# Kernel optimization log

Hardware: AMD Instinct MI355X
Metric: run time of the kernel (lower is better)

The kernel has to match this reference:

```python
import jax, jax.numpy as jnp
import numpy as np

N_NODES = 100000
N_EDGES = 1600000
D_IN = 128
D_OUT = 32
DROP_P = 0.6
NEG_SLOPE = 0.2


def setup_inputs() -> dict:
    key = jax.random.key(0)
    ks = jax.random.split(key, 10)
    x = jax.random.normal(ks[0], (N_NODES, D_IN), dtype=jnp.float32)
    edge_index = jax.random.randint(ks[1], (2, N_EDGES), 0, N_NODES, dtype=jnp.int32)
    drop_u = jax.random.uniform(ks[2], (N_NODES, D_IN), dtype=jnp.float32)
    s = 1.0 / np.sqrt(D_IN)
    W_src = jax.random.normal(ks[3], (D_IN, D_OUT), dtype=jnp.float32) * s
    W_dst = jax.random.normal(ks[4], (D_IN, D_OUT), dtype=jnp.float32) * s
    att_src = jax.random.normal(ks[5], (D_OUT,), dtype=jnp.float32) * s
    att_dst = jax.random.normal(ks[6], (D_OUT,), dtype=jnp.float32) * s
    bias_gat = jax.random.normal(ks[7], (D_OUT,), dtype=jnp.float32) * 0.01
    W_lin = jax.random.normal(ks[8], (D_OUT, D_OUT), dtype=jnp.float32) / np.sqrt(D_OUT)
    b_lin = jax.random.normal(ks[9], (D_OUT,), dtype=jnp.float32) * 0.01
    return {"x": x, "edge_index": edge_index, "drop_u": drop_u,
            "W_src": W_src, "W_dst": W_dst, "att_src": att_src,
            "att_dst": att_dst, "bias_gat": bias_gat,
            "W_lin": W_lin, "b_lin": b_lin}


def reference(x, edge_index, drop_u, W_src, W_dst, att_src, att_dst,
              bias_gat, W_lin, b_lin):
    n = x.shape[0]
    # F.dropout(x, p=0.6, training=True) with deterministic uniform draws
    keep = (drop_u > DROP_P).astype(x.dtype)
    xd = x * keep / (1.0 - DROP_P)

    # GATConv (heads=1): separate src/dst linear maps
    h_src = xd @ W_src                      # [N, D_OUT]
    h_dst = xd @ W_dst                      # [N, D_OUT]
    a_src = h_src @ att_src                 # [N]
    a_dst = h_dst @ att_dst                 # [N]

    # add_self_loops=True (PyG default)
    loops = jnp.arange(n, dtype=edge_index.dtype)
    src = jnp.concatenate([edge_index[0], loops])   # [E+N]
    dst = jnp.concatenate([edge_index[1], loops])   # [E+N]

    e = a_src[src] + a_dst[dst]                      # per-edge raw score
    e = jnp.where(e > 0, e, NEG_SLOPE * e)           # leaky_relu(0.2)

    # segment softmax over destination-node neighborhoods
    e_max = jax.ops.segment_max(e, dst, num_segments=n)  # every node has a self loop
    e_exp = jnp.exp(e - e_max[dst])
    denom = jax.ops.segment_sum(e_exp, dst, num_segments=n)
    alpha = e_exp / denom[dst]                       # [E+N]

    # scatter-add aggregation of weighted source features
    msg = h_src[src] * alpha[:, None]                # [E+N, D_OUT]
    out = jax.ops.segment_sum(msg, dst, num_segments=n) + bias_gat

    # residual linear + relu + log_softmax
    out = out + out @ W_lin + b_lin
    out = jax.nn.relu(out)
    logp = jax.nn.log_softmax(out, axis=1)
    return logp, alpha
```

## Files before the change

### kernel.cpp

```cpp
#include <hip/hip_runtime.h>
#include <hip/hip_bf16.h>
#include <math.h>

#define D_IN   128
#define D_OUT  32
#define NEG_SLOPE 0.2f
#define DROP_P 0.6f
#define KEEP_SCALE 2.5f

#define NPB     128
#define NB      782
#define CAPB    2816
#define CHUNK   4096
#define BT      512
#define EPT     8
#define SRC_BITS 17
#define SRC_MASK ((1u << SRC_BITS) - 1)

#define SLICES  4
#define NPS     32
#define CAPS    896
#define EPT3    11

typedef __attribute__((ext_vector_type(8))) short fragAB;
typedef __attribute__((ext_vector_type(4))) float fragCD;

__device__ __forceinline__ void atomicMaxF(float* addr, float v) {
    if (v >= 0.0f) atomicMax((int*)addr, __float_as_int(v));
    else           atomicMin((unsigned int*)addr, __float_as_uint(v));
}

__device__ __forceinline__ unsigned pack_bf16(float lo, float hi) {
    __hip_bfloat16 l = __float2bfloat16(lo);
    __hip_bfloat16 h = __float2bfloat16(hi);
    unsigned short lb, hb;
    __builtin_memcpy(&lb, &l, 2);
    __builtin_memcpy(&hb, &h, 2);
    return (unsigned)lb | ((unsigned)hb << 16);
}

__device__ __forceinline__ unsigned short f2bf(float f) {
    __hip_bfloat16 h = __float2bfloat16(f);
    unsigned short u;
    __builtin_memcpy(&u, &h, 2);
    return u;
}

__global__ void k_fold(const float* __restrict__ W_src, const float* __restrict__ W_dst,
                       const float* __restrict__ att_src, const float* __restrict__ att_dst,
                       float* __restrict__ v_src, float* __restrict__ v_dst,
                       int* __restrict__ gcur, uint4* __restrict__ wfrag) {
    int gi = blockIdx.x * blockDim.x + threadIdx.x;
    if (gi < NB) gcur[gi] = gi * CAPB;
    if (gi < 512) {
        int tile = gi >> 8;
        int kb   = (gi >> 6) & 3;
        int lane = gi & 63;
        int grp = lane >> 4, col = lane & 15;
        int kbase = kb * 32 + grp * 8;
        int cidx  = tile * 16 + col;
        unsigned o0 = pack_bf16(W_src[(kbase + 0) * D_OUT + cidx], W_src[(kbase + 1) * D_OUT + cidx]);
        unsigned o1 = pack_bf16(W_src[(kbase + 2) * D_OUT + cidx], W_src[(kbase + 3) * D_OUT + cidx]);
        unsigned o2 = pack_bf16(W_src[(kbase + 4) * D_OUT + cidx], W_src[(kbase + 5) * D_OUT + cidx]);
        unsigned o3 = pack_bf16(W_src[(kbase + 6) * D_OUT + cidx], W_src[(kbase + 7) * D_OUT + cidx]);
        wfrag[gi] = make_uint4(o0, o1, o2, o3);
    }
    if (blockIdx.x == 0) {
        int k = threadIdx.x;
        if (k < D_IN) {
            float s = 0.f, d = 0.f;
            #pragma unroll
            for (int c = 0; c < D_OUT; ++c) {
                s += W_src[k * D_OUT + c] * att_src[c];
                d += W_dst[k * D_OUT + c] * att_dst[c];
            }
            v_src[k] = s;
            v_dst[k] = d;
        }
    }
}

__global__ __launch_bounds__(256) void k_nodes_mfma(
    const float* __restrict__ x, const float* __restrict__ drop_u,
    const uint4* __restrict__ wfrag,
    const float* __restrict__ v_src, const float* __restrict__ v_dst,
    unsigned short* __restrict__ h_bf16,
    float* __restrict__ a_src, float* __restrict__ a_dst,
    int n)
{
    int tid  = threadIdx.x;
    int wv   = tid >> 6;
    int lane = tid & 63;
    int nbase = blockIdx.x * 64 + wv * 16;
    int row = lane & 15, grp = lane >> 4;

    int arow_raw = nbase + row;
    bool aact = arow_raw < n;
    int arow = aact ? arow_raw : (n - 1);
    const float* xr = x      + (size_t)arow * D_IN;
    const float* dr = drop_u + (size_t)arow * D_IN;

    fragCD c0 = {0.f, 0.f, 0.f, 0.f};
    fragCD c1 = {0.f, 0.f, 0.f, 0.f};
    float ps = 0.f, pd = 0.f;

    #pragma unroll
    for (int kb = 0; kb < 4; ++kb) {
        int k0 = kb * 32 + grp * 8;
        float4 xa = *(const float4*)(xr + k0);
        float4 xb = *(const float4*)(xr + k0 + 4);
        float4 da = *(const float4*)(dr + k0);
        float4 db = *(const float4*)(dr + k0 + 4);
        float f0 = da.x > DROP_P ? xa.x * KEEP_SCALE : 0.f;
        float f1 = da.y > DROP_P ? xa.y * KEEP_SCALE : 0.f;
        float f2 = da.z > DROP_P ? xa.z * KEEP_SCALE : 0.f;
        float f3 = da.w > DROP_P ? xa.w * KEEP_SCALE : 0.f;
        float f4 = db.x > DROP_P ? xb.x * KEEP_SCALE : 0.f;
        float f5 = db.y > DROP_P ? xb.y * KEEP_SCALE : 0.f;
        float f6 = db.z > DROP_P ? xb.z * KEEP_SCALE : 0.f;
        float f7 = db.w > DROP_P ? xb.w * KEEP_SCALE : 0.f;

        float4 vs1 = *(const float4*)(v_src + k0);
        float4 vs2 = *(const float4*)(v_src + k0 + 4);
        float4 vd1 = *(const float4*)(v_dst + k0);
        float4 vd2 = *(const float4*)(v_dst + k0 + 4);
        ps += f0 * vs1.x + f1 * vs1.y + f2 * vs1.z + f3 * vs1.w
            + f4 * vs2.x + f5 * vs2.y + f6 * vs2.z + f7 * vs2.w;
        pd += f0 * vd1.x + f1 * vd1.y + f2 * vd1.z + f3 * vd1.w
            + f4 * vd2.x + f5 * vd2.y + f6 * vd2.z + f7 * vd2.w;

        union { unsigned u[4]; fragAB v; } af;
        af.u[0] = pack_bf16(f0, f1);
        af.u[1] = pack_bf16(f2, f3);
        af.u[2] = pack_bf16(f4, f5);
        af.u[3] = pack_bf16(f6, f7);

        fragAB b0 = *reinterpret_cast<const fragAB*>(&wfrag[kb * 64 + lane]);
        fragAB b1 = *reinterpret_cast<const fragAB*>(&wfrag[256 + kb * 64 + lane]);
        c0 = __builtin_amdgcn_mfma_f32_16x16x32_bf16(af.v, b0, c0, 0, 0, 0);
        c1 = __builtin_amdgcn_mfma_f32_16x16x32_bf16(af.v, b1, c1, 0, 0, 0);
    }

    ps += __shfl_xor(ps, 16); ps += __shfl_xor(ps, 32);
    pd += __shfl_xor(pd, 16); pd += __shfl_xor(pd, 32);
    if (grp == 0 && aact) { a_src[arow_raw] = ps; a_dst[arow_raw] = pd; }

    #pragma unroll
    for (int r = 0; r < 4; ++r) {
        int onode = nbase + grp * 4 + r;
        if (onode < n) {
            h_bf16[(size_t)onode * D_OUT + row]      = f2bf(c0[r]);
            h_bf16[(size_t)onode * D_OUT + 16 + row] = f2bf(c1[r]);
        }
    }
}

__global__ __launch_bounds__(256) void k_nodes(
    const float* __restrict__ x, const float* __restrict__ drop_u,
    const float* __restrict__ W_src,
    const float* __restrict__ v_src, const float* __restrict__ v_dst,
    float* __restrict__ h_src, float* __restrict__ a_src, float* __restrict__ a_dst,
    float* __restrict__ e_max, float* __restrict__ denom,
    float* __restrict__ agg, int n, int init_aux)
{
    int gt = blockIdx.x * 256 + threadIdx.x;
    int node_raw = gt >> 2;
    int sub = gt & 3;
    bool act = node_raw < n;
    int node = act ? node_raw : (n - 1);

    const float4* xr4 = (const float4*)(x      + (size_t)node * D_IN) + sub * 8;
    const float4* dr4 = (const float4*)(drop_u + (size_t)node * D_IN) + sub * 8;
    const float*  wb  = W_src + sub * 32 * D_OUT;
    const float4* vsp = (const float4*)v_src + sub * 8;
    const float4* vdp = (const float4*)v_dst + sub * 8;

    float4 xv[8];
    #pragma unroll
    for (int q = 0; q < 8; ++q) {
        float4 xl = xr4[q];
        float4 dl = dr4[q];
        xv[q].x = dl.x > DROP_P ? xl.x * KEEP_SCALE : 0.f;
        xv[q].y = dl.y > DROP_P ? xl.y * KEEP_SCALE : 0.f;
        xv[q].z = dl.z > DROP_P ? xl.z * KEEP_SCALE : 0.f;
        xv[q].w = dl.w > DROP_P ? xl.w * KEEP_SCALE : 0.f;
    }

    float acc[D_OUT];
    #pragma unroll
    for (int c = 0; c < D_OUT; ++c) acc[c] = 0.f;
    float ps = 0.f, pd = 0.f;

    #pragma unroll
    for (int q = 0; q < 8; ++q) {
        float4 vs4 = vsp[q];
        float4 vd4 = vdp[q];
        ps += xv[q].x * vs4.x + xv[q].y * vs4.y + xv[q].z * vs4.z + xv[q].w * vs4.w;
        pd += xv[q].x * vd4.x + xv[q].y * vd4.y + xv[q].z * vd4.z + xv[q].w * vd4.w;
        #pragma unroll
        for (int kk = 0; kk < 4; ++kk) {
            float xk = (kk == 0) ? xv[q].x : (kk == 1) ? xv[q].y : (kk == 2) ? xv[q].z : xv[q].w;
            const float4* wrow = (const float4*)(wb + (q * 4 + kk) * D_OUT);
            #pragma unroll
            for (int c4 = 0; c4 < 8; ++c4) {
                float4 w = wrow[c4];
                acc[c4 * 4 + 0] += xk * w.x;
                acc[c4 * 4 + 1] += xk * w.y;
                acc[c4 * 4 + 2] += xk * w.z;
                acc[c4 * 4 + 3] += xk * w.w;
            }
        }
    }

    #pragma unroll
    for (int c = 0; c < D_OUT; ++c) {
        acc[c] += __shfl_xor(acc[c], 1);
        acc[c] += __shfl_xor(acc[c], 2);
    }
    ps += __shfl_xor(ps, 1); ps += __shfl_xor(ps, 2);
    pd += __shfl_xor(pd, 1); pd += __shfl_xor(pd, 2);

    if (act) {
        if (sub == 0) {
            a_src[node] = ps;
            a_dst[node] = pd;
            if (init_aux) { e_max[node] = -3.0e38f; denom[node] = 0.f; }
        }
        float o[8];
        if (sub == 0) {
            #pragma unroll
            for (int i = 0; i < 8; ++i) o[i] = acc[i];
        } else if (sub == 1) {
            #pragma unroll
            for (int i = 0; i < 8; ++i) o[i] = acc[8 + i];
        } else if (sub == 2) {
            #pragma unroll
            for (int i = 0; i < 8; ++i) o[i] = acc[16 + i];
        } else {
            #pragma unroll
            for (int i = 0; i < 8; ++i) o[i] = acc[24 + i];
        }
        float4* hb = (float4*)(h_src + (size_t)node * D_OUT + sub * 8);
        hb[0] = make_float4(o[0], o[1], o[2], o[3]);
        hb[1] = make_float4(o[4], o[5], o[6], o[7]);
        if (init_aux) {
            float4* ab = (float4*)(agg + (size_t)node * D_OUT + sub * 8);
            ab[0] = make_float4(0.f, 0.f, 0.f, 0.f);
            ab[1] = make_float4(0.f, 0.f, 0.f, 0.f);
        }
    }
}

__global__ __launch_bounds__(BT) void k_binsort(
    const int* __restrict__ ei, int E, int n,
    const float* __restrict__ a_src, const float* __restrict__ a_dst,
    int* __restrict__ gcur, uint2* __restrict__ binned)
{
    __shared__ int A[1024], B[1024];
    __shared__ int excl[NB + 1];
    __shared__ int lcur[NB];
    __shared__ int gpos[NB];
    __shared__ uint2 stage[CHUNK];
    __shared__ unsigned short sbk[CHUNK];

    int tid = threadIdx.x;
    int T   = E + n;
    int base = blockIdx.x * CHUNK;

    for (int k = tid; k < 1024; k += BT) A[k] = 0;
    __syncthreads();

    uint2 rec[EPT];
    int   bk [EPT];
    #pragma unroll
    for (int e = 0; e < EPT; ++e) {
        int i = base + e * BT + tid;
        if (i < T) {
            int s, d;
            if (i < E) { s = ei[i]; d = ei[E + i]; }
            else       { s = d = i - E; }
            int b    = d >> 7;
            int drel = d & 127;
            float sc = a_src[s] + a_dst[d];
            sc = sc > 0.f ? sc : NEG_SLOPE * sc;
            rec[e].x = (unsigned)s | ((unsigned)drel << SRC_BITS);
            rec[e].y = __float_as_uint(expf(sc));
            bk[e]  = b;
            atomicAdd(&A[b], 1);
        } else bk[e] = -1;
    }
    __syncthreads();

    int* cur = A; int* nxt = B;
    for (int off = 1; off < 1024; off <<= 1) {
        for (int k = tid; k < 1024; k += BT) {
            int v = cur[k];
            if (k >= off) v += cur[k - off];
            nxt[k] = v;
        }
        __syncthreads();
        int* t = cur; cur = nxt; nxt = t;
    }

    for (int b = tid; b < NB; b += BT) {
        int e0 = b ? cur[b - 1] : 0;
        excl[b] = e0;
        lcur[b] = e0;
        int c = cur[b] - e0;
        gpos[b] = c ? atomicAdd(&gcur[b], c) : 0;
    }
    if (tid == 0) excl[NB] = cur[NB - 1];
    __syncthreads();

    #pragma unroll
    for (int e = 0; e < EPT; ++e) {
        if (bk[e] >= 0) {
            int slot = atomicAdd(&lcur[bk[e]], 1);
            stage[slot] = rec[e];
            sbk[slot]   = (unsigned short)bk[e];
        }
    }
    __syncthreads();

    int tot = excl[NB];
    for (int j = tid; j < tot; j += BT) {
        int b = sbk[j];
        unsigned gd = (unsigned)(gpos[b] + (j - excl[b]));
        if (gd < (unsigned)(b + 1) * CAPB)
            binned[gd] = stage[j];
    }
}

__global__ __launch_bounds__(256) void k_bucket3(
    const uint2* __restrict__ binned, const int* __restrict__ gcur,
    const unsigned short* __restrict__ h_bf16,
    const float* __restrict__ bias_gat, const float* __restrict__ W_lin,
    const float* __restrict__ b_lin,
    float* __restrict__ inv_out,
    float* __restrict__ io, int n)
{
    __shared__ uint2 grp[CAPS];
    __shared__ int A[NPS];
    __shared__ int ends[NPS];
    __shared__ int ncur[NPS];
    __shared__ float Wl[D_OUT * D_OUT];
    __shared__ float ul[8][D_OUT];

    int tid   = threadIdx.x;
    int lin   = (blockIdx.x & 7) * ((NB * SLICES) >> 3) + (blockIdx.x >> 3);
    int b     = lin >> 2;
    int slice = lin & 3;
    int n0    = b * NPB + slice * NPS;
    int nn    = n - n0; if (nn > NPS) nn = NPS;
    if (nn <= 0) return;

    for (int i = tid; i < D_OUT * D_OUT; i += 256) Wl[i] = W_lin[i];
    if (tid < NPS) A[tid] = 0;
    __syncthreads();

    int cnt = gcur[b] - b * CAPB;
    if (cnt > CAPB) cnt = CAPB;
    const uint2* src = binned + (size_t)b * CAPB;

    uint2 rr[EPT3];
    #pragma unroll
    for (int e = 0; e < EPT3; ++e) {
        int j = tid + e * 256;
        if (j < cnt) {
            uint2 r = src[j];
            rr[e] = r;
            int drel = r.x >> SRC_BITS;
            if ((drel >> 5) == slice) atomicAdd(&A[drel & 31], 1);
        }
    }
    __syncthreads();

    if (tid < NPS) {
        int v = A[tid];
        #pragma unroll
        for (int off = 1; off < NPS; off <<= 1) {
            int u = __shfl_up(v, off, NPS);
            if (tid >= off) v += u;
        }
        ends[tid] = v;
        ncur[tid] = v - A[tid];
    }
    __syncthreads();

    #pragma unroll
    for (int e = 0; e < EPT3; ++e) {
        int j = tid + e * 256;
        if (j < cnt) {
            uint2 r = rr[e];
            int drel = r.x >> SRC_BITS;
            if ((drel >> 5) == slice) {
                int pos = atomicAdd(&ncur[drel & 31], 1);
                if (pos < CAPS) grp[pos] = make_uint2(r.x & SRC_MASK, r.y);
            }
        }
    }
    __syncthreads();

    int g = tid >> 5, lane = tid & 31;
    float bg = bias_gat[lane];
    float bl = b_lin[lane];

    for (int nr = g; nr < nn; nr += 8) {
        int st = nr ? ends[nr - 1] : 0;
        int en = ends[nr];
        if (st > CAPS) st = CAPS;
        if (en > CAPS) en = CAPS;
        int node = n0 + nr;

        float ss = 0.f;
        for (int j = st + lane; j < en; j += 32)
            ss += __uint_as_float(grp[j].y);
        #pragma unroll
        for (int o = 16; o; o >>= 1) ss += __shfl_xor(ss, o);
        float inv = 1.0f / ss;
        if (lane == 0) inv_out[node] = inv;

        float acc0 = 0.f, acc1 = 0.f, acc2 = 0.f, acc3 = 0.f;
        float acc4 = 0.f, acc5 = 0.f, acc6 = 0.f, acc7 = 0.f;
        int j = st;
        for (; j + 7 < en; j += 8) {
            uint2 p0 = grp[j],     p1 = grp[j + 1];
            uint2 p2 = grp[j + 2], p3 = grp[j + 3];
            uint2 p4 = grp[j + 4], p5 = grp[j + 5];
            uint2 p6 = grp[j + 6], p7 = grp[j + 7];
            float h0 = __uint_as_float((unsigned)h_bf16[(p0.x << 5) + lane] << 16);
            float h1 = __uint_as_float((unsigned)h_bf16[(p1.x << 5) + lane] << 16);
            float h2 = __uint_as_float((unsigned)h_bf16[(p2.x << 5) + lane] << 16);
            float h3 = __uint_as_float((unsigned)h_bf16[(p3.x << 5) + lane] << 16);
            float h4 = __uint_as_float((unsigned)h_bf16[(p4.x << 5) + lane] << 16);
            float h5 = __uint_as_float((unsigned)h_bf16[(p5.x << 5) + lane] << 16);
            float h6 = __uint_as_float((unsigned)h_bf16[(p6.x << 5) + lane] << 16);
            float h7 = __uint_as_float((unsigned)h_bf16[(p7.x << 5) + lane] << 16);
            acc0 += h0 * __uint_as_float(p0.y);
            acc1 += h1 * __uint_as_float(p1.y);
            acc2 += h2 * __uint_as_float(p2.y);
            acc3 += h3 * __uint_as_float(p3.y);
            acc4 += h4 * __uint_as_float(p4.y);
            acc5 += h5 * __uint_as_float(p5.y);
            acc6 += h6 * __uint_as_float(p6.y);
            acc7 += h7 * __uint_as_float(p7.y);
        }
        for (; j < en; ++j) {
            uint2 p = grp[j];
            acc0 += __uint_as_float((unsigned)h_bf16[(p.x << 5) + lane] << 16)
                  * __uint_as_float(p.y);
        }

        float u = (((acc0 + acc1) + (acc2 + acc3)) + ((acc4 + acc5) + (acc6 + acc7))) * inv + bg;
        ul[g][lane] = u;
        float r2 = u + bl;
        #pragma unroll 8
        for (int k = 0; k < D_OUT; ++k)
            r2 += ul[g][k] * Wl[k * D_OUT + lane];
        r2 = fmaxf(r2, 0.f);

        float mm = r2;
        #pragma unroll
        for (int o = 16; o; o >>= 1) mm = fmaxf(mm, __shfl_xor(mm, o));
        float e2 = expf(r2 - mm);
        float s2 = e2;
        #pragma unroll
        for (int o = 16; o; o >>= 1) s2 += __shfl_xor(s2, o);
        io[(size_t)node * D_OUT + lane] = r2 - mm - logf(s2);
    }
}

__global__ void k_alpha(const int* __restrict__ ei, int E, int n,
                        const float* __restrict__ a_src, const float* __restrict__ a_dst,
                        const float* __restrict__ inv,
                        float* __restrict__ alpha_out)
{
    int i = blockIdx.x * blockDim.x + threadIdx.x;
    int T = E + n;
    if (i >= T) return;
    int s, d;
    if (i < E) { s = ei[i]; d = ei[E + i]; }
    else       { s = d = i - E; }
    float e = a_src[s] + a_dst[d];
    e = e > 0.f ? e : NEG_SLOPE * e;
    alpha_out[i] = expf(e) * inv[d];
}

__global__ void k_edge_score(const int* __restrict__ ei, int E, int n,
                             const float* __restrict__ a_src, const float* __restrict__ a_dst,
                             float* __restrict__ score_out, float* __restrict__ e_max)
{
    int total = E + n;
    int i = blockIdx.x * blockDim.x + threadIdx.x;
    if (i >= total) return;
    int s, d;
    if (i < E) { s = ei[i]; d = ei[E + i]; }
    else       { s = d = i - E; }
    float e = a_src[s] + a_dst[d];
    e = e > 0.f ? e : NEG_SLOPE * e;
    score_out[i] = e;
    atomicMaxF(&e_max[d], e);
}

__global__ void k_edge_exp(const int* __restrict__ ei, int E, int n,
                           const float* __restrict__ e_max,
                           float* __restrict__ score_io, float* __restrict__ denom)
{
    int total = E + n;
    int i = blockIdx.x * blockDim.x + threadIdx.x;
    if (i >= total) return;
    int d = (i < E) ? ei[E + i] : (i - E);
    float ex = expf(score_io[i] - e_max[d]);
    score_io[i] = ex;
    atomicAdd(&denom[d], ex);
}

__global__ __launch_bounds__(256) void k_edge_agg(
    const int* __restrict__ ei, int E, int n,
    const float* __restrict__ h_src, const float* __restrict__ denom,
    float* __restrict__ alpha_io, float* __restrict__ agg)
{
    int tid  = threadIdx.x;
    int loc  = tid >> 5;
    int lane = tid & 31;
    int i = blockIdx.x * 8 + loc;
    int total = E + n;
    if (i >= total) return;
    int s, d;
    if (i < E) { s = ei[i]; d = ei[E + i]; }
    else       { s = d = i - E; }
    float alpha = alpha_io[i] / denom[d];
    if (lane == 0) alpha_io[i] = alpha;
    float m = h_src[(size_t)s * D_OUT + lane] * alpha;
    atomicAdd(&agg[(size_t)d * D_OUT + lane], m);
}

__global__ __launch_bounds__(256) void k_final(
    const float* __restrict__ bias_gat, const float* __restrict__ W_lin,
    const float* __restrict__ b_lin, float* __restrict__ io, int n)
{
    __shared__ float Wl[D_OUT * D_OUT];
    __shared__ float ul[8][D_OUT];

    int tid = threadIdx.x;
    for (int i = tid; i < D_OUT * D_OUT; i += 256) Wl[i] = W_lin[i];
    __syncthreads();

    int loc  = tid >> 5;
    int lane = tid & 31;
    int node = blockIdx.x * 8 + loc;

    float u = 0.f;
    if (node < n) u = io[(size_t)node * D_OUT + lane] + bias_gat[lane];
    ul[loc][lane] = u;
    __syncthreads();

    float r = u + b_lin[lane];
    #pragma unroll 8
    for (int k = 0; k < D_OUT; ++k)
        r += ul[loc][k] * Wl[k * D_OUT + lane];
    r = fmaxf(r, 0.f);

    float m = r;
    #pragma unroll
    for (int off = 16; off; off >>= 1) m = fmaxf(m, __shfl_xor(m, off));
    float ex = expf(r - m);
    float ssum = ex;
    #pragma unroll
    for (int off = 16; off; off >>= 1) ssum += __shfl_xor(ssum, off);
    float logp = r - m - logf(ssum);

    if (node < n) io[(size_t)node * D_OUT + lane] = logp;
}

extern "C" void kernel_launch(void* const* d_in, const int* in_sizes, int n_in,
                              void* d_out, int out_size, void* d_ws, size_t ws_size,
                              hipStream_t stream)
{
    const float* x        = (const float*)d_in[0];
    const int*   ei       = (const int*)  d_in[1];
    const float* drop_u   = (const float*)d_in[2];
    const float* W_src    = (const float*)d_in[3];
    const float* W_dst    = (const float*)d_in[4];
    const float* att_src  = (const float*)d_in[5];
    const float* att_dst  = (const float*)d_in[6];
    const float* bias_gat = (const float*)d_in[7];
    const float* W_lin    = (const float*)d_in[8];
    const float* b_lin    = (const float*)d_in[9];

    const int N = in_sizes[0] / D_IN;
    const int E = in_sizes[1] / 2;
    const int total = E + N;

    float* ws = (float*)d_ws;

    float* v_src = ws;
    float* v_dst = ws + 128;
    float* h_src = ws + 256;
    unsigned short* h_bf16 = (unsigned short*)h_src;
    float* a_src = h_src + (size_t)N * D_OUT;
    float* a_dst = a_src + N;
    float* m_buf = a_dst + N;
    float* i_buf = m_buf + N;

    size_t idx = 256 + (size_t)N * D_OUT + 4 * (size_t)N;
    int* gcur = (int*)(ws + idx);       idx += NB + 2;
    idx = (idx + 3) & ~(size_t)3;
    uint4* wfrag = (uint4*)(ws + idx);  idx += 2048;
    uint2* binned = (uint2*)(ws + idx); idx += 2 * (size_t)NB * CAPB;
    size_t need_bytes = idx * sizeof(float);

    float* logp_out  = (float*)d_out;
    float* alpha_out = (float*)d_out + (size_t)N * D_OUT;

    int mfmaBlocks = (N + 63) / 64;
    int nodeBlocks = (int)(((size_t)N * 4 + 255) / 256);
    int nodeBlocks8 = (N + 7) / 8;
    int eb = (total + 255) / 256;

    bool fits = (ws_size >= need_bytes) && (N < (1 << SRC_BITS)) && (N <= NB * NPB);

    if (fits) {
        k_fold<<<7, 128, 0, stream>>>(W_src, W_dst, att_src, att_dst,
                                      v_src, v_dst, gcur, wfrag);
        k_nodes_mfma<<<mfmaBlocks, 256, 0, stream>>>(x, drop_u, wfrag, v_src, v_dst,
                                                     h_bf16, a_src, a_dst, N);
        int nchunk = (total + CHUNK - 1) / CHUNK;
        k_binsort<<<nchunk, BT, 0, stream>>>(ei, E, N, a_src, a_dst, gcur, binned);
        k_bucket3<<<NB * SLICES, 256, 0, stream>>>(binned, gcur, h_bf16,
                                                   bias_gat, W_lin, b_lin,
                                                   i_buf, logp_out, N);
        k_alpha<<<eb, 256, 0, stream>>>(ei, E, N, a_src, a_dst, i_buf, alpha_out);
    } else {
        k_fold<<<7, 128, 0, stream>>>(W_src, W_dst, att_src, att_dst,
                                      v_src, v_dst, gcur, wfrag);
        k_nodes<<<nodeBlocks, 256, 0, stream>>>(x, drop_u, W_src, v_src, v_dst,
                                                h_src, a_src, a_dst,
                                                m_buf, i_buf, logp_out, N, 1);
        k_edge_score<<<eb, 256, 0, stream>>>(ei, E, N, a_src, a_dst, alpha_out, m_buf);
        k_edge_exp<<<eb, 256, 0, stream>>>(ei, E, N, m_buf, alpha_out, i_buf);
        int aggBlocks = (total + 7) / 8;
        k_edge_agg<<<aggBlocks, 256, 0, stream>>>(ei, E, N, h_src, i_buf, alpha_out, logp_out);
        k_final<<<nodeBlocks8, 256, 0, stream>>>(bias_gat, W_lin, b_lin, logp_out, N);
    }
}
```

Before: 128.8 us.

## Shrink destination bins to 64 nodes and drop per-slice bucket filtering

Destination bins go from 128 to 64 nodes, so there are 1563 bins with 1536-record capacity. The aggregation kernel now runs one block per bin instead of four slice blocks that each read the whole 128-node bin and discarded three quarters of it. The goal is to stop re-reading binned edge records and to simplify local bucketing. In exchange, the binsort kernel uses smaller chunks and a longer shared-memory prefix scan over 2048 bins, and more global bin-counter atomics are spread over more bins.

```diff
diff --git a/kernel.cpp b/kernel.cpp
--- a/kernel.cpp
+++ b/kernel.cpp
@@ -8,19 +8,16 @@
 #define DROP_P 0.6f
 #define KEEP_SCALE 2.5f
 
-#define NPB     128
-#define NB      782
-#define CAPB    2816
-#define CHUNK   4096
+#define NPB     64
+#define NB      1563
+#define NBPAD   2048
+#define CAPB    1536
+#define CHUNK   2048
 #define BT      512
-#define EPT     8
+#define EPT     4
 #define SRC_BITS 17
 #define SRC_MASK ((1u << SRC_BITS) - 1)
-
-#define SLICES  4
-#define NPS     32
-#define CAPS    896
-#define EPT3    11
+#define EPT3    6
 
 typedef __attribute__((ext_vector_type(8))) short fragAB;
 typedef __attribute__((ext_vector_type(4))) float fragCD;
@@ -256,7 +253,7 @@
     const float* __restrict__ a_src, const float* __restrict__ a_dst,
     int* __restrict__ gcur, uint2* __restrict__ binned)
 {
-    __shared__ int A[1024], B[1024];
+    __shared__ int A[NBPAD], B[NBPAD];
     __shared__ int excl[NB + 1];
     __shared__ int lcur[NB];
     __shared__ int gpos[NB];
@@ -267,7 +264,7 @@
     int T   = E + n;
     int base = blockIdx.x * CHUNK;
 
-    for (int k = tid; k < 1024; k += BT) A[k] = 0;
+    for (int k = tid; k < NBPAD; k += BT) A[k] = 0;
     __syncthreads();
 
     uint2 rec[EPT];
@@ -279,8 +276,8 @@
             int s, d;
             if (i < E) { s = ei[i]; d = ei[E + i]; }
             else       { s = d = i - E; }
-            int b    = d >> 7;
-            int drel = d & 127;
+            int b    = d >> 6;
+            int drel = d & 63;
             float sc = a_src[s] + a_dst[d];
             sc = sc > 0.f ? sc : NEG_SLOPE * sc;
             rec[e].x = (unsigned)s | ((unsigned)drel << SRC_BITS);
@@ -292,8 +289,8 @@
     __syncthreads();
 
     int* cur = A; int* nxt = B;
-    for (int off = 1; off < 1024; off <<= 1) {
-        for (int k = tid; k < 1024; k += BT) {
+    for (int off = 1; off < NBPAD; off <<= 1) {
+        for (int k = tid; k < NBPAD; k += BT) {
             int v = cur[k];
             if (k >= off) v += cur[k - off];
             nxt[k] = v;
@@ -331,7 +328,7 @@
     }
 }
 
-__global__ __launch_bounds__(256) void k_bucket3(
+__global__ __launch_bounds__(256) void k_bucket4(
     const uint2* __restrict__ binned, const int* __restrict__ gcur,
     const unsigned short* __restrict__ h_bf16,
     const float* __restrict__ bias_gat, const float* __restrict__ W_lin,
@@ -339,23 +336,21 @@
     float* __restrict__ inv_out,
     float* __restrict__ io, int n)
 {
-    __shared__ uint2 grp[CAPS];
-    __shared__ int A[NPS];
-    __shared__ int ends[NPS];
-    __shared__ int ncur[NPS];
+    __shared__ uint2 grp[CAPB];
+    __shared__ int A[NPB];
+    __shared__ int ends[NPB];
+    __shared__ int ncur[NPB];
     __shared__ float Wl[D_OUT * D_OUT];
     __shared__ float ul[8][D_OUT];
 
-    int tid   = threadIdx.x;
-    int lin   = (blockIdx.x & 7) * ((NB * SLICES) >> 3) + (blockIdx.x >> 3);
-    int b     = lin >> 2;
-    int slice = lin & 3;
-    int n0    = b * NPB + slice * NPS;
-    int nn    = n - n0; if (nn > NPS) nn = NPS;
+    int tid = threadIdx.x;
+    int b   = blockIdx.x;
+    int n0  = b * NPB;
+    int nn  = n - n0; if (nn > NPB) nn = NPB;
     if (nn <= 0) return;
 
     for (int i = tid; i < D_OUT * D_OUT; i += 256) Wl[i] = W_lin[i];
-    if (tid < NPS) A[tid] = 0;
+    if (tid < NPB) A[tid] = 0;
     __syncthreads();
 
     int cnt = gcur[b] - b * CAPB;
@@ -369,17 +364,16 @@
         if (j < cnt) {
             uint2 r = src[j];
             rr[e] = r;
-            int drel = r.x >> SRC_BITS;
-            if ((drel >> 5) == slice) atomicAdd(&A[drel & 31], 1);
-        }
-    }
-    __syncthreads();
-
-    if (tid < NPS) {
+            atomicAdd(&A[r.x >> SRC_BITS], 1);
+        }
+    }
+    __syncthreads();
+
+    if (tid < NPB) {
         int v = A[tid];
         #pragma unroll
-        for (int off = 1; off < NPS; off <<= 1) {
-            int u = __shfl_up(v, off, NPS);
+        for (int off = 1; off < NPB; off <<= 1) {
+            int u = __shfl_up(v, off);
             if (tid >= off) v += u;
         }
         ends[tid] = v;
@@ -392,11 +386,8 @@
         int j = tid + e * 256;
         if (j < cnt) {
             uint2 r = rr[e];
-            int drel = r.x >> SRC_BITS;
-            if ((drel >> 5) == slice) {
-                int pos = atomicAdd(&ncur[drel & 31], 1);
-                if (pos < CAPS) grp[pos] = make_uint2(r.x & SRC_MASK, r.y);
-            }
+            int pos = atomicAdd(&ncur[r.x >> SRC_BITS], 1);
+            grp[pos] = make_uint2(r.x & SRC_MASK, r.y);
         }
     }
     __syncthreads();
@@ -408,8 +399,6 @@
     for (int nr = g; nr < nn; nr += 8) {
         int st = nr ? ends[nr - 1] : 0;
         int en = ends[nr];
-        if (st > CAPS) st = CAPS;
-        if (en > CAPS) en = CAPS;
         int node = n0 + nr;
 
         float ss = 0.f;
@@ -621,19 +610,19 @@
     bool fits = (ws_size >= need_bytes) && (N < (1 << SRC_BITS)) && (N <= NB * NPB);
 
     if (fits) {
-        k_fold<<<7, 128, 0, stream>>>(W_src, W_dst, att_src, att_dst,
-                                      v_src, v_dst, gcur, wfrag);
+        k_fold<<<(NB + 127) / 128, 128, 0, stream>>>(W_src, W_dst, att_src, att_dst,
+                                                     v_src, v_dst, gcur, wfrag);
         k_nodes_mfma<<<mfmaBlocks, 256, 0, stream>>>(x, drop_u, wfrag, v_src, v_dst,
                                                      h_bf16, a_src, a_dst, N);
         int nchunk = (total + CHUNK - 1) / CHUNK;
         k_binsort<<<nchunk, BT, 0, stream>>>(ei, E, N, a_src, a_dst, gcur, binned);
-        k_bucket3<<<NB * SLICES, 256, 0, stream>>>(binned, gcur, h_bf16,
-                                                   bias_gat, W_lin, b_lin,
-                                                   i_buf, logp_out, N);
+        k_bucket4<<<NB, 256, 0, stream>>>(binned, gcur, h_bf16,
+                                          bias_gat, W_lin, b_lin,
+                                          i_buf, logp_out, N);
         k_alpha<<<eb, 256, 0, stream>>>(ei, E, N, a_src, a_dst, i_buf, alpha_out);
     } else {
-        k_fold<<<7, 128, 0, stream>>>(W_src, W_dst, att_src, att_dst,
-                                      v_src, v_dst, gcur, wfrag);
+        k_fold<<<(NB + 127) / 128, 128, 0, stream>>>(W_src, W_dst, att_src, att_dst,
+                                                     v_src, v_dst, gcur, wfrag);
         k_nodes<<<nodeBlocks, 256, 0, stream>>>(x, drop_u, W_src, v_src, v_dst,
                                                 h_src, a_src, a_dst,
                                                 m_buf, i_buf, logp_out, N, 1);
```

New measurement: 145.4 us. 1.13x slower.
